# Kernel optimization log

Measured on AMD Instinct MI355X. Metric: run time of the kernel, lower is better.

Reference implementation:

```python
import jax, jax.numpy as jnp
import numpy as np


def setup_inputs() -> dict:
    key = jax.random.key(0)
    B, D, H, W = 4, 2, 2048, 2048
    # displacement field in voxels (B, D, H, W); ~1 voxel displacements
    phi = jax.random.normal(key, (B, D, H, W), dtype=jnp.float32)
    return {"phi": phi}


def reference(phi):
    """Count/splat ones through a displacement field with bilinear weights
    and 'wrap' (periodic) boundary conditions.

    phi : (B, 2, H, W) displacement in voxels -> count : (B, 1, H, W)
    """
    B, D, H, W = phi.shape
    ii = jnp.arange(H, dtype=phi.dtype)[:, None]   # (H,1)
    jj = jnp.arange(W, dtype=phi.dtype)[None, :]   # (1,W)
    # sample positions = identity + displacement
    x = ii + phi[:, 0]                             # (B,H,W) along dim 0
    y = jj + phi[:, 1]                             # (B,H,W) along dim 1

    x0 = jnp.floor(x)
    y0 = jnp.floor(y)
    wx1 = x - x0                                   # fractional weights
    wy1 = y - y0
    wx0 = 1.0 - wx1
    wy0 = 1.0 - wy1

    # periodic (wrap) boundary: indices mod size
    ix0 = jnp.mod(x0.astype(jnp.int32), H)
    ix1 = jnp.mod(ix0 + 1, H)
    iy0 = jnp.mod(y0.astype(jnp.int32), W)
    iy1 = jnp.mod(iy0 + 1, W)

    boff = (jnp.arange(B, dtype=jnp.int32) * (H * W))[:, None, None]  # batch offset

    out = jnp.zeros((B * H * W,), dtype=phi.dtype)

    def splat(acc, ix, iy, w):
        idx = (boff + ix * W + iy).ravel()
        return acc.at[idx].add(w.ravel())

    out = splat(out, ix0, iy0, wx0 * wy0)
    out = splat(out, ix0, iy1, wx0 * wy1)
    out = splat(out, ix1, iy0, wx1 * wy0)
    out = splat(out, ix1, iy1, wx1 * wy1)

    return out.reshape(B, 1, H, W)
```

## Files before the change

### kernel.cpp

```cpp
#include <hip/hip_runtime.h>

constexpr int H = 2048, W = 2048;
constexpr int HW = H * W;
constexpr int OUTW = 56;
constexpr int NCH = (W + OUTW - 1) / OUTW;
constexpr int RB  = 8;
constexpr int WPB = 4;
constexpr int ROWSPB = RB * WPB;
constexpr int NSRC = RB + 6;

__global__ __launch_bounds__(256, 3)
void splat_gather8o(const float* __restrict__ phi, float* __restrict__ out,
                    unsigned char* __restrict__ flags) {
    int wid  = threadIdx.x >> 6;
    int lane = threadIdx.x & 63;

    const int rgPerImg = H / ROWSPB;
    int bid = blockIdx.x;
    int b   = bid / (NCH * rgPerImg);
    int rem = bid - b * (NCH * rgPerImg);
    int c0i = rem / rgPerImg;
    int rg  = rem - c0i * rgPerImg;
    int r0  = rg * ROWSPB + wid * RB;
    int c0  = c0i * OUTW;

    const float* phiB = phi + (size_t)b * 2 * HW;
    float* outb = out + (size_t)b * HW;

    int scu = c0 - 4 + lane;
    int scw = scu & (W - 1);
    bool ownedCol = (lane >= 4) && (lane < 4 + OUTW) && (scu < W);

    float dxv[NSRC], dyv[NSRC];
    #pragma unroll
    for (int t = 0; t < NSRC; ++t) {
        int srow = (r0 + t - 3) & (H - 1);
        dxv[t] = phiB[(size_t)srow * W + scw];
        dyv[t] = phiB[(size_t)HW + (size_t)srow * W + scw];
    }
    #pragma unroll
    for (int t = 0; t < NSRC; ++t)
        asm volatile("" : "+v"(dxv[t]), "+v"(dyv[t]));

    float slot[RB][7];
    #pragma unroll
    for (int m = 0; m < RB; ++m)
        #pragma unroll
        for (int k = 0; k < 7; ++k) slot[m][k] = 0.0f;

    #pragma unroll
    for (int t = 0; t < NSRC; ++t) {
        float dx = dxv[t], dy = dyv[t];
        bool valid = (__builtin_fabsf(dx) < 3.0f) && (__builtin_fabsf(dy) < 3.0f);
        float dyM = valid ? dy : 16384.0f;

        float ct[7];
        #pragma unroll
        for (int k = 0; k < 7; ++k) {
            float d = dyM - (float)(k - 3);
            ct[k] = __builtin_fmaxf(1.0f - __builtin_fabsf(d), 0.0f);
        }
        #pragma unroll
        for (int k = 0; k < 7; ++k)
            asm volatile("" : "+v"(ct[k]));

        #pragma unroll
        for (int m = 0; m < RB; ++m) {
            if (t - m < 0 || t - m > 6) continue;
            float dist = dx + (float)(t - 3 - m);
            float rw = __builtin_fmaxf(1.0f - __builtin_fabsf(dist), 0.0f);
            #pragma unroll
            for (int k = 0; k < 7; ++k)
                slot[m][k] = __builtin_fmaf(rw, ct[k], slot[m][k]);
        }

        if (t >= 3 && t < 3 + RB) {
            bool need = (!valid) && ownedCol;
            unsigned long long mask = __ballot(need);
            if (lane == 0) {
                int srow = (r0 + t - 3) & (H - 1);
                flags[(size_t)(b * H + srow) * NCH + c0i] = (mask != 0ull) ? 1 : 0;
            }
        }
    }

    #pragma unroll
    for (int m = 0; m < RB; ++m) {
        float v = 0.0f;
        #pragma unroll
        for (int k = 0; k < 7; ++k)
            v += __shfl(slot[m][k], lane - (k - 3));
        if (ownedCol)
            outb[(size_t)(r0 + m) * W + scu] = v;
    }
}

__global__ __launch_bounds__(256)
void flush_flagged(const float* __restrict__ phi, const unsigned char* __restrict__ flags,
                   float* __restrict__ out) {
    int wid  = threadIdx.x >> 6;
    int lane = threadIdx.x & 63;
    unsigned base = ((unsigned)blockIdx.x * WPB + (unsigned)wid) * 16u;

    unsigned char f = (lane < 16) ? flags[base + (unsigned)lane] : (unsigned char)0;
    unsigned long long mask = __ballot(f != 0);

    while (mask) {
        int bit = (int)(__ffsll((long long)mask) - 1);
        mask &= mask - 1ull;
        unsigned chunk = base + (unsigned)bit;

        int c0i  = (int)(chunk % (unsigned)NCH);
        unsigned bs = chunk / (unsigned)NCH;
        int srow = (int)(bs & (H - 1));
        int b    = (int)(bs >> 11);

        int col = c0i * OUTW + lane;
        if (lane < OUTW && col < W) {
            const float* phiB = phi + (size_t)b * 2 * HW;
            float dx = phiB[(size_t)srow * W + col];
            float dy = phiB[(size_t)HW + (size_t)srow * W + col];
            if (!((__builtin_fabsf(dx) < 3.0f) && (__builtin_fabsf(dy) < 3.0f))) {
                float* outb = out + (size_t)b * HW;
                float x = (float)srow + dx;
                float y = (float)col + dy;
                float x0 = floorf(x), y0 = floorf(y);
                float wx1 = x - x0, wx0 = 1.0f - wx1;
                float wy1 = y - y0, wy0 = 1.0f - wy1;
                int gx0 = ((int)x0) & (H - 1);
                int gx1 = (gx0 + 1) & (H - 1);
                int gy0 = ((int)y0) & (W - 1);
                int gy1 = (gy0 + 1) & (W - 1);
                atomicAdd(outb + (size_t)gx0 * W + gy0, wx0 * wy0);
                atomicAdd(outb + (size_t)gx0 * W + gy1, wx0 * wy1);
                atomicAdd(outb + (size_t)gx1 * W + gy0, wx1 * wy0);
                atomicAdd(outb + (size_t)gx1 * W + gy1, wx1 * wy1);
            }
        }
    }
}

extern "C" void kernel_launch(void* const* d_in, const int* in_sizes, int n_in,
                              void* d_out, int out_size, void* d_ws, size_t ws_size,
                              hipStream_t stream) {
    const float* phi = (const float*)d_in[0];
    float* out = (float*)d_out;
    unsigned char* flags = (unsigned char*)d_ws;

    int B = out_size / HW;
    int grid = B * NCH * (H / ROWSPB);
    splat_gather8o<<<grid, 256, 0, stream>>>(phi, out, flags);

    long long nChunks = (long long)B * H * NCH;
    int grid2 = (int)(nChunks / (WPB * 16));
    flush_flagged<<<grid2, 256, 0, stream>>>(phi, flags, out);
}
```

Baseline: 82.70 us.

## Accumulate bilinear splat weights in packed fp16 pairs

Converts the per-row column weights and slot accumulators from fp32 to packed half2 vectors, so the inner FMA loop runs as packed fp16 operations with roughly half the instruction and register count. Occupancy is raised from 3 to 4 workgroups per CU to use the freed registers. The cost is reduced precision in the accumulated weights: sums of up to 7 contributions are rounded to fp16, which may exceed the tolerance. Shuffles now move packed pairs and extract the needed half.

```diff
diff --git a/kernel.cpp b/kernel.cpp
--- a/kernel.cpp
+++ b/kernel.cpp
@@ -9,8 +9,11 @@
 constexpr int ROWSPB = RB * WPB;
 constexpr int NSRC = RB + 6;
 
-__global__ __launch_bounds__(256, 3)
-void splat_gather8o(const float* __restrict__ phi, float* __restrict__ out,
+typedef _Float16 f16;
+typedef f16 f16x2 __attribute__((ext_vector_type(2)));
+
+__global__ __launch_bounds__(256, 4)
+void splat_gather8h(const float* __restrict__ phi, float* __restrict__ out,
                     unsigned char* __restrict__ flags) {
     int wid  = threadIdx.x >> 6;
     int lane = threadIdx.x & 63;
@@ -42,11 +45,11 @@
     for (int t = 0; t < NSRC; ++t)
         asm volatile("" : "+v"(dxv[t]), "+v"(dyv[t]));
 
-    float slot[RB][7];
+    f16x2 slot[RB][4];
     #pragma unroll
     for (int m = 0; m < RB; ++m)
         #pragma unroll
-        for (int k = 0; k < 7; ++k) slot[m][k] = 0.0f;
+        for (int p = 0; p < 4; ++p) slot[m][p] = (f16x2)((f16)0.0);
 
     #pragma unroll
     for (int t = 0; t < NSRC; ++t) {
@@ -54,24 +57,28 @@
         bool valid = (__builtin_fabsf(dx) < 3.0f) && (__builtin_fabsf(dy) < 3.0f);
         float dyM = valid ? dy : 16384.0f;
 
-        float ct[7];
+        f16 dyh = (f16)dyM;
+        f16x2 dy2 = {dyh, dyh};
+        f16x2 ct[4];
         #pragma unroll
-        for (int k = 0; k < 7; ++k) {
-            float d = dyM - (float)(k - 3);
-            ct[k] = __builtin_fmaxf(1.0f - __builtin_fabsf(d), 0.0f);
+        for (int p = 0; p < 4; ++p) {
+            const f16x2 koff = {(f16)(2 * p - 3), (f16)(2 * p - 2)};
+            f16x2 d  = dy2 - koff;
+            f16x2 a  = __builtin_elementwise_abs(d);
+            f16x2 tt = (f16x2)((f16)1.0) - a;
+            ct[p] = __builtin_elementwise_max(tt, (f16x2)((f16)0.0));
         }
-        #pragma unroll
-        for (int k = 0; k < 7; ++k)
-            asm volatile("" : "+v"(ct[k]));
 
         #pragma unroll
         for (int m = 0; m < RB; ++m) {
             if (t - m < 0 || t - m > 6) continue;
             float dist = dx + (float)(t - 3 - m);
-            float rw = __builtin_fmaxf(1.0f - __builtin_fabsf(dist), 0.0f);
+            float rwf = __builtin_fmaxf(1.0f - __builtin_fabsf(dist), 0.0f);
+            f16 rwh = (f16)rwf;
+            f16x2 rw2 = {rwh, rwh};
             #pragma unroll
-            for (int k = 0; k < 7; ++k)
-                slot[m][k] = __builtin_fmaf(rw, ct[k], slot[m][k]);
+            for (int p = 0; p < 4; ++p)
+                slot[m][p] = __builtin_elementwise_fma(rw2, ct[p], slot[m][p]);
         }
 
         if (t >= 3 && t < 3 + RB) {
@@ -88,8 +95,17 @@
     for (int m = 0; m < RB; ++m) {
         float v = 0.0f;
         #pragma unroll
-        for (int k = 0; k < 7; ++k)
-            v += __shfl(slot[m][k], lane - (k - 3));
+        for (int p = 0; p < 4; ++p) {
+            int s = __builtin_bit_cast(int, slot[m][p]);
+            int rlo = __shfl(s, lane - (2 * p - 3));
+            f16x2 vlo = __builtin_bit_cast(f16x2, rlo);
+            v += (float)vlo.x;
+            if (p < 3) {
+                int rhi = __shfl(s, lane - (2 * p - 2));
+                f16x2 vhi = __builtin_bit_cast(f16x2, rhi);
+                v += (float)vhi.y;
+            }
+        }
         if (ownedCol)
             outb[(size_t)(r0 + m) * W + scu] = v;
     }
@@ -149,7 +165,7 @@
 
     int B = out_size / HW;
     int grid = B * NCH * (H / ROWSPB);
-    splat_gather8o<<<grid, 256, 0, stream>>>(phi, out, flags);
+    splat_gather8h<<<grid, 256, 0, stream>>>(phi, out, flags);
 
     long long nChunks = (long long)B * H * NCH;
     int grid2 = (int)(nChunks / (WPB * 16));
```

After: 89.84 us. +8.6%, slower.
